# Kernel optimization log

Hardware: AMD Instinct MI355X
Metric: run time of the kernel (lower is better)

## Reference

```python
import jax, jax.numpy as jnp
import numpy as np

THETA = 10000.0

def _rope(t):
    # lucidrains-style interleaved rotary over the FULL last dim (dim=hidden_size)
    T, d = t.shape[-2], t.shape[-1]
    freqs = 1.0 / (THETA ** (jnp.arange(0, d, 2, dtype=jnp.float32) / d))  # (d/2,)
    ang = jnp.arange(T, dtype=jnp.float32)[:, None] * freqs[None, :]       # (T, d/2)
    ang = jnp.repeat(ang, 2, axis=-1)                                      # (T, d) interleaved
    cos, sin = jnp.cos(ang), jnp.sin(ang)
    x = t.reshape(t.shape[:-1] + (d // 2, 2))
    x1, x2 = x[..., 0], x[..., 1]
    rot = jnp.stack([-x2, x1], axis=-1).reshape(t.shape)  # rotate_half, interleaved pairs
    return t * cos + rot * sin


def setup_inputs() -> dict:
    key = jax.random.key(0)
    ks = jax.random.split(key, 5)
    B, T, C = 4, 2048, 1024
    s = 0.02
    return {
        "x":  jax.random.normal(ks[0], (B, T, C), dtype=jnp.float32),
        "Wq": jax.random.normal(ks[1], (C, C), dtype=jnp.float32) * s,
        "bq": jnp.zeros((C,), dtype=jnp.float32),
        "Wk": jax.random.normal(ks[2], (C, C), dtype=jnp.float32) * s,
        "bk": jnp.zeros((C,), dtype=jnp.float32),
        "Wv": jax.random.normal(ks[3], (C, C), dtype=jnp.float32) * s,
        "bv": jnp.zeros((C,), dtype=jnp.float32),
        "Wf": jax.random.normal(ks[4], (C, C), dtype=jnp.float32) * s,
        "bf": jnp.zeros((C,), dtype=jnp.float32),
    }


def reference(x, Wq, bq, Wk, bk, Wv, bv, Wf, bf):
    B, T, C = x.shape
    Q = _rope(x @ Wq.T + bq)
    K = _rope(x @ Wk.T + bk)
    V = x @ Wv.T + bv
    # scores [B,T,T]; _get_D(gamma=1, T) is exactly a causal lower-triangular mask
    A = jnp.einsum('btd,bsd->bts', Q, K) / jnp.sqrt(jnp.float32(C))
    causal = jnp.tril(jnp.ones((T, T), dtype=bool))
    A = jnp.where(causal, A, -jnp.inf)
    A = jax.nn.softmax(A, axis=-1)
    out = jnp.einsum('bts,bsd->btd', A, V)
    return out @ Wf.T + bf
```

## Files before the change

### kernel.cpp

```cpp
#include <hip/hip_runtime.h>
#include <math.h>


#define AS1(p) ((__attribute__((address_space(1))) void*)(p))
#define AS3(p) ((__attribute__((address_space(3))) void*)(p))

typedef __attribute__((ext_vector_type(8))) short bf16x8;
typedef __attribute__((ext_vector_type(4))) float f32x4;

__device__ __forceinline__ unsigned short f2bf(float f) {
  unsigned int u = __float_as_uint(f);
  u += 0x7fffu + ((u >> 16) & 1u);
  return (unsigned short)(u >> 16);
}

__global__ __launch_bounds__(256) void cast_all(
    const float* __restrict__ x, const float* __restrict__ Wq,
    const float* __restrict__ Wk, const float* __restrict__ Wv,
    const float* __restrict__ Wf,
    unsigned short* __restrict__ xb, unsigned short* __restrict__ Wqb,
    unsigned short* __restrict__ Wkb, unsigned short* __restrict__ Wvb,
    unsigned short* __restrict__ Wfb) {
  int i = blockIdx.x * 256 + threadIdx.x;
  const float* src; unsigned short* dst; int off;
  if (i < 2097152) { src = x; dst = xb; off = i; }
  else {
    int j = i - 2097152;
    int w = j >> 18; off = j & 262143;
    src = (w == 0) ? Wq : (w == 1) ? Wk : (w == 2) ? Wv : Wf;
    dst = (w == 0) ? Wqb : (w == 1) ? Wkb : (w == 2) ? Wvb : Wfb;
  }
  float4 f = ((const float4*)src)[off];
  ushort4 o;
  o.x = f2bf(f.x); o.y = f2bf(f.y); o.z = f2bf(f.z); o.w = f2bf(f.w);
  ((ushort4*)dst)[off] = o;
}

__device__ __forceinline__ void gemm_core(const unsigned short* __restrict__ At, long long lda,
                                          const unsigned short* __restrict__ Bt, long long ldb,
                                          int K, f32x4 (&acc)[4][4],
                                          unsigned short* As, unsigned short* Bs) {
  const int tid  = threadIdx.x;
  const int lane = tid & 63;
  const int w    = tid >> 6;
  const int wm   = (w & 1) << 6;
  const int wn   = (w >> 1) << 6;
  const int fr   = lane & 15;
  const int fq   = lane >> 4;
  const int srow = tid >> 2;
  const int scol = (tid & 3) << 3;
  const int lg   = ((tid & 3) ^ ((srow >> 1) & 3)) << 3;
  const unsigned short* a0 = At + (long long)srow * lda + lg;
  const unsigned short* a1 = At + (long long)(srow + 64) * lda + lg;
  const unsigned short* b0 = Bt + (long long)srow * ldb + lg;
  const unsigned short* b1 = Bt + (long long)(srow + 64) * ldb + lg;
  unsigned short* As0 = As + srow * 32 + scol;
  unsigned short* As1 = As + (srow + 64) * 32 + scol;
  unsigned short* Bs0 = Bs + srow * 32 + scol;
  unsigned short* Bs1 = Bs + (srow + 64) * 32 + scol;
  const int pg = (fq ^ ((fr >> 1) & 3)) << 3;
  for (int k0 = 0; k0 < K; k0 += 32) {
    __builtin_amdgcn_global_load_lds(AS1(a0 + k0), AS3(As0), 16, 0, 0);
    __builtin_amdgcn_global_load_lds(AS1(a1 + k0), AS3(As1), 16, 0, 0);
    __builtin_amdgcn_global_load_lds(AS1(b0 + k0), AS3(Bs0), 16, 0, 0);
    __builtin_amdgcn_global_load_lds(AS1(b1 + k0), AS3(Bs1), 16, 0, 0);
    __syncthreads();
    bf16x8 af[4], bfr[4];
#pragma unroll
    for (int i = 0; i < 4; i++)
      af[i] = *(const bf16x8*)(As + (wm + i * 16 + fr) * 32 + pg);
#pragma unroll
    for (int i = 0; i < 4; i++)
      bfr[i] = *(const bf16x8*)(Bs + (wn + i * 16 + fr) * 32 + pg);
#pragma unroll
    for (int mi = 0; mi < 4; mi++)
#pragma unroll
      for (int ni = 0; ni < 4; ni++)
        acc[mi][ni] = __builtin_amdgcn_mfma_f32_16x16x32_bf16(af[mi], bfr[ni], acc[mi][ni], 0, 0, 0);
    __syncthreads();
  }
}

__device__ __forceinline__ void repack_store_mi(unsigned short (&vals)[4][4],
                                                unsigned short* sh, int mi,
                                                int m0, int n0, long long ldo,
                                                unsigned short* __restrict__ Out) {
  const int tid = threadIdx.x, lane = tid & 63, w = tid >> 6;
  const int half = w & 1, wn = (w >> 1) << 6;
  const int cl = lane & 15, q4 = lane >> 4;
  const int lr = half * 16 + q4 * 4;
#pragma unroll
  for (int ni = 0; ni < 4; ni++)
#pragma unroll
    for (int rr = 0; rr < 4; rr++)
      sh[(lr + rr) * 132 + wn + ni * 16 + cl] = vals[ni][rr];
  __syncthreads();
#pragma unroll
  for (int it = 0; it < 2; ++it) {
    int row = (tid >> 4) + it * 16;
    int c8 = (tid & 15) << 3;
    bf16x8 v = *(const bf16x8*)(sh + row * 132 + c8);
    int gr = m0 + (row < 16 ? mi * 16 + row : 48 + mi * 16 + row);
    *(bf16x8*)(Out + (long long)gr * ldo + n0 + c8) = v;
  }
  __syncthreads();
}

__global__ __launch_bounds__(256) void proj_rope(
    const unsigned short* __restrict__ xb,
    const unsigned short* __restrict__ Wq, const unsigned short* __restrict__ Wk,
    const unsigned short* __restrict__ Wv,
    const float* __restrict__ bq, const float* __restrict__ bk, const float* __restrict__ bv,
    unsigned short* __restrict__ Q, unsigned short* __restrict__ Ko,
    unsigned short* __restrict__ Vt) {
  __shared__ unsigned short sh[8192];
  const int which = blockIdx.z;
  const int tid = threadIdx.x, lane = tid & 63, w = tid >> 6;
  const int wm = (w & 1) << 6, wn = (w >> 1) << 6;
  const int cl = lane & 15, q4 = lane >> 4;

  f32x4 acc[4][4];
#pragma unroll
  for (int i = 0; i < 4; i++)
#pragma unroll
    for (int j = 0; j < 4; j++)
#pragma unroll
      for (int k = 0; k < 4; k++) acc[i][j][k] = 0.0f;

  if (which == 2) {
    const int s0g = blockIdx.x * 128;
    const int d0 = blockIdx.y * 128;
    gemm_core(Wv + (long long)d0 * 1024, 1024, xb + (long long)s0g * 1024, 1024,
              1024, acc, sh, sh + 4096);
    const int b = s0g >> 11;
    const int sloc = s0g & 2047;
    unsigned short* Outb = Vt + (long long)b * 1024 * 2048;
#pragma unroll
    for (int mi = 0; mi < 4; mi++) {
      unsigned short vals[4][4];
#pragma unroll
      for (int rr = 0; rr < 4; rr++) {
        const float b_ = bv[d0 + wm + mi * 16 + q4 * 4 + rr];
#pragma unroll
        for (int ni = 0; ni < 4; ni++)
          vals[ni][rr] = f2bf(acc[mi][ni][rr] + b_);
      }
      repack_store_mi(vals, sh, mi, d0, sloc, 2048, Outb);
    }
    return;
  }

  const int m0 = blockIdx.x * 128;
  const int n0 = blockIdx.y * 128;
  const unsigned short* W = which == 0 ? Wq : Wk;
  const float* bias = which == 0 ? bq : bk;
  unsigned short* Out = which == 0 ? Q : Ko;

  gemm_core(xb + (long long)m0 * 1024, 1024, W + (long long)n0 * 1024, 1024, 1024, acc, sh, sh + 4096);

  const float NEG_L2T_512 = -0.025952563239354392f;
  const float INV2PI = 0.15915494309189535f;
  float freqn[4];
#pragma unroll
  for (int ni = 0; ni < 4; ni++) {
    int gn = n0 + wn + ni * 16 + cl;
    freqn[ni] = exp2f(NEG_L2T_512 * (float)(gn >> 1));
  }
#pragma unroll
  for (int mi = 0; mi < 4; mi++) {
    unsigned short vals[4][4];
    const int t0 = (m0 & 2047) + wm + mi * 16 + q4 * 4;
#pragma unroll
    for (int ni = 0; ni < 4; ni++) {
      const int gn = n0 + wn + ni * 16 + cl;
#pragma unroll
      for (int rr = 0; rr < 4; rr++) {
        float v = acc[mi][ni][rr] + bias[gn];
        float partner = __shfl_xor(v, 1, 64);
        float ang = (float)(t0 + rr) * freqn[ni];
        float rev = ang * INV2PI;
        rev = rev - floorf(rev);
        float c = __builtin_amdgcn_cosf(rev);
        float s = __builtin_amdgcn_sinf(rev);
        v = v * c + ((gn & 1) ? partner : -partner) * s;
        vals[ni][rr] = f2bf(v);
      }
    }
    repack_store_mi(vals, sh, mi, m0, n0, 1024, Out);
  }
}

__global__ __launch_bounds__(256) void score_exp(const unsigned short* __restrict__ Q,
                                                 const unsigned short* __restrict__ Kk,
                                                 unsigned short* __restrict__ P,
                                                 float* __restrict__ row_sum) {
  __shared__ unsigned short sh[8192];
  const int bx = blockIdx.x;
  int i = (int)((sqrtf(8.0f * (float)bx + 1.0f) - 1.0f) * 0.5f);
  while ((i + 1) * (i + 2) / 2 <= bx) ++i;
  while (i * (i + 1) / 2 > bx) --i;
  const int j = bx - i * (i + 1) / 2;
  const int b = blockIdx.z;
  const int m0 = i * 128, n0 = j * 128;
  const unsigned short* Qb = Q + (long long)b * 2048 * 1024;
  const unsigned short* Kb = Kk + (long long)b * 2048 * 1024;
  unsigned short* Pb = P + (long long)b * 2048 * 2048;
  float* rs = row_sum + b * 2048;

  f32x4 acc[4][4];
#pragma unroll
  for (int ii = 0; ii < 4; ii++)
#pragma unroll
    for (int jj = 0; jj < 4; jj++)
#pragma unroll
      for (int k = 0; k < 4; k++) acc[ii][jj][k] = 0.0f;

  gemm_core(Qb + (long long)m0 * 1024, 1024, Kb + (long long)n0 * 1024, 1024, 1024, acc, sh, sh + 4096);

  const int tid = threadIdx.x, lane = tid & 63, w = tid >> 6;
  const int wm = (w & 1) << 6, wn = (w >> 1) << 6;
  const int cl = lane & 15, q4 = lane >> 4;
  const bool diag = (i == j);
#pragma unroll
  for (int mi = 0; mi < 4; mi++) {
    unsigned short vals[4][4];
    float rsum[4] = {0.f, 0.f, 0.f, 0.f};
#pragma unroll
    for (int ni = 0; ni < 4; ni++) {
      const int gn = n0 + wn + ni * 16 + cl;
#pragma unroll
      for (int rr = 0; rr < 4; rr++) {
        const int gm = m0 + wm + mi * 16 + q4 * 4 + rr;
        float e = (diag && gn > gm) ? 0.0f : __expf(acc[mi][ni][rr] * 0.03125f);
        vals[ni][rr] = f2bf(e);
        rsum[rr] += e;
      }
    }
#pragma unroll
    for (int rr = 0; rr < 4; rr++) {
#pragma unroll
      for (int off = 1; off < 16; off <<= 1) rsum[rr] += __shfl_xor(rsum[rr], off, 64);
    }
    if (cl == 0) {
      const int gm = m0 + wm + mi * 16 + q4 * 4;
#pragma unroll
      for (int rr = 0; rr < 4; rr++) atomicAdd(&rs[gm + rr], rsum[rr]);
    }
    repack_store_mi(vals, sh, mi, m0, n0, 2048, Pb);
  }
}

__global__ __launch_bounds__(256) void pv_gemm(const unsigned short* __restrict__ P,
                                               const unsigned short* __restrict__ Vt,
                                               const float* __restrict__ row_sum,
                                               unsigned short* __restrict__ O) {
  __shared__ unsigned short sh[8192];
  const int b = blockIdx.z;
  const int mt = 15 - blockIdx.x;
  const int m0 = mt * 128;
  const int n0 = blockIdx.y * 128;
  const unsigned short* Pb = P + (long long)b * 2048 * 2048;
  const unsigned short* Vb = Vt + (long long)b * 1024 * 2048;
  const float* rs = row_sum + b * 2048;
  const int K = m0 + 128;

  f32x4 acc[4][4];
#pragma unroll
  for (int i = 0; i < 4; i++)
#pragma unroll
    for (int j = 0; j < 4; j++)
#pragma unroll
      for (int k = 0; k < 4; k++) acc[i][j][k] = 0.0f;

  gemm_core(Pb + (long long)m0 * 2048, 2048, Vb + (long long)n0 * 2048, 2048, K, acc, sh, sh + 4096);

  const int tid = threadIdx.x, lane = tid & 63, w = tid >> 6;
  const int wm = (w & 1) << 6;
  const int q4 = lane >> 4;
#pragma unroll
  for (int mi = 0; mi < 4; mi++) {
    unsigned short vals[4][4];
    float inv[4];
    const int gm0 = m0 + wm + mi * 16 + q4 * 4;
#pragma unroll
    for (int rr = 0; rr < 4; rr++) inv[rr] = 1.0f / rs[gm0 + rr];
#pragma unroll
    for (int ni = 0; ni < 4; ni++)
#pragma unroll
      for (int rr = 0; rr < 4; rr++)
        vals[ni][rr] = f2bf(acc[mi][ni][rr] * inv[rr]);
    repack_store_mi(vals, sh, mi, m0, n0, 1024, O + (long long)b * 2048 * 1024);
  }
}

__global__ __launch_bounds__(256) void final_gemm(const unsigned short* __restrict__ O,
                                                  const unsigned short* __restrict__ Wf,
                                                  const float* __restrict__ bf_,
                                                  float* __restrict__ out) {
  __shared__ unsigned short sh[8448];
  float* shf = (float*)sh;
  const int m0 = blockIdx.x * 128;
  const int n0 = blockIdx.y * 128;

  f32x4 acc[4][4];
#pragma unroll
  for (int i = 0; i < 4; i++)
#pragma unroll
    for (int j = 0; j < 4; j++)
#pragma unroll
      for (int k = 0; k < 4; k++) acc[i][j][k] = 0.0f;

  gemm_core(O + (long long)m0 * 1024, 1024, Wf + (long long)n0 * 1024, 1024, 1024, acc, sh, sh + 4096);

  const int tid = threadIdx.x, lane = tid & 63, w = tid >> 6;
  const int half = w & 1, wn = (w >> 1) << 6;
  const int cl = lane & 15, q4 = lane >> 4;
  const int lr = half * 16 + q4 * 4;
#pragma unroll
  for (int mi = 0; mi < 4; mi++) {
#pragma unroll
    for (int ni = 0; ni < 4; ni++)
#pragma unroll
      for (int rr = 0; rr < 4; rr++)
        shf[(lr + rr) * 130 + wn + ni * 16 + cl] = acc[mi][ni][rr] + bf_[n0 + wn + ni * 16 + cl];
    __syncthreads();
    {
      int row = tid >> 3;
      int c4 = (tid & 7) << 4;
      int gr = m0 + (row < 16 ? mi * 16 + row : 48 + mi * 16 + row);
      float* dst = out + (long long)gr * 1024 + n0 + c4;
      const float* srcp = shf + row * 130 + c4;
#pragma unroll
      for (int j = 0; j < 4; j++)
        ((float4*)dst)[j] = ((const float4*)srcp)[j];
    }
    __syncthreads();
  }
}

extern "C" void kernel_launch(void* const* d_in, const int* in_sizes, int n_in,
                              void* d_out, int out_size, void* d_ws, size_t ws_size,
                              hipStream_t stream) {
  (void)in_sizes; (void)n_in; (void)out_size; (void)ws_size;
  const float* x   = (const float*)d_in[0];
  const float* Wq  = (const float*)d_in[1];
  const float* bq  = (const float*)d_in[2];
  const float* Wk  = (const float*)d_in[3];
  const float* bk  = (const float*)d_in[4];
  const float* Wv  = (const float*)d_in[5];
  const float* bv  = (const float*)d_in[6];
  const float* Wf  = (const float*)d_in[7];
  const float* bf_ = (const float*)d_in[8];
  float* out = (float*)d_out;

  char* ws = (char*)d_ws;
  const size_t MB = 1024 * 1024;
  unsigned short* xb  = (unsigned short*)(ws);
  unsigned short* Wqb = (unsigned short*)(ws + 16 * MB);
  unsigned short* Wkb = (unsigned short*)(ws + 18 * MB);
  unsigned short* Wvb = (unsigned short*)(ws + 20 * MB);
  unsigned short* Wfb = (unsigned short*)(ws + 22 * MB);
  unsigned short* Qb  = (unsigned short*)(ws + 24 * MB);
  unsigned short* Kb  = (unsigned short*)(ws + 40 * MB);
  unsigned short* Vtb = (unsigned short*)(ws + 56 * MB);
  unsigned short* Ob  = (unsigned short*)(ws + 72 * MB);
  unsigned short* Pb  = (unsigned short*)(ws + 88 * MB);
  float*          rsum= (float*)(ws + 120 * MB);

  dim3 blk(256);
  hipMemsetAsync(rsum, 0, 8192 * sizeof(float), stream);
  cast_all<<<dim3(3145728 / 256), blk, 0, stream>>>(x, Wq, Wk, Wv, Wf, xb, Wqb, Wkb, Wvb, Wfb);
  proj_rope<<<dim3(64, 8, 3), blk, 0, stream>>>(xb, Wqb, Wkb, Wvb, bq, bk, bv, Qb, Kb, Vtb);
  score_exp<<<dim3(136, 1, 4), blk, 0, stream>>>(Qb, Kb, Pb, rsum);
  pv_gemm<<<dim3(16, 8, 4), blk, 0, stream>>>(Pb, Vtb, rsum, Ob);
  final_gemm<<<dim3(64, 8), blk, 0, stream>>>(Ob, Wfb, bf_, out);
}
```

Measured before the change: 299.1 us.

## Replace projection and output GEMM cores with 8-wave 128x256 pipelined core

Adds a new 512-thread GEMM core with 128x256 tiles, K-step 64, double-buffered direct global-to-LDS loads, XOR-swizzled LDS reads, and phased MFMA interleaving with setprio and barriers. The QKV projection and final output GEMM switch to it with larger tiles and new epilogues that stage results through LDS for coalesced stores. The aim is to raise MFMA utilisation and hide memory latency in these GEMMs. In exchange it uses much more LDS per block and many barriers, and it launches fewer blocks.

```diff
diff --git a/kernel.cpp b/kernel.cpp
--- a/kernel.cpp
+++ b/kernel.cpp
@@ -106,17 +106,134 @@
   __syncthreads();
 }
 
-__global__ __launch_bounds__(256) void proj_rope(
+__device__ __forceinline__ void core8(
+    const unsigned short* __restrict__ A, long long lda,
+    const unsigned short* __restrict__ B, long long ldb,
+    int nkt, f32x4 (&acc)[4][4], unsigned short* lds) {
+  const int tid  = threadIdx.x;
+  const int lane = tid & 63;
+  const int w    = tid >> 6;
+  const int wr   = w >> 2;
+  const int wc   = w & 3;
+  const int fr   = lane & 15;
+  const int fq   = lane >> 4;
+  const int rsw0 = (fq ^ (fr & 7)) << 3;
+  const int rsw1 = ((4 + fq) ^ (fr & 7)) << 3;
+  const int sr   = tid >> 3;
+  const int kswz = ((tid & 7) ^ (sr & 7)) << 3;
+  const unsigned short* Asrc = A + (long long)sr * lda + kswz;
+  const unsigned short* Bsrc = B + (long long)sr * ldb + kswz;
+  unsigned short* ldsw = lds + tid * 8;
+
+  auto stageA = [&](int b_, int kt_) {
+    const unsigned short* s0 = Asrc + (long long)kt_ * 64;
+    __builtin_amdgcn_global_load_lds(AS1(s0),            AS3(ldsw + b_ * 24576),         16, 0, 0);
+    __builtin_amdgcn_global_load_lds(AS1(s0 + 64 * lda), AS3(ldsw + b_ * 24576 + 4096),  16, 0, 0);
+  };
+  auto stageB = [&](int b_, int kt_) {
+    const unsigned short* s0 = Bsrc + (long long)kt_ * 64;
+    __builtin_amdgcn_global_load_lds(AS1(s0),             AS3(ldsw + b_ * 24576 + 8192),  16, 0, 0);
+    __builtin_amdgcn_global_load_lds(AS1(s0 + 64 * ldb),  AS3(ldsw + b_ * 24576 + 12288), 16, 0, 0);
+    __builtin_amdgcn_global_load_lds(AS1(s0 + 128 * ldb), AS3(ldsw + b_ * 24576 + 16384), 16, 0, 0);
+    __builtin_amdgcn_global_load_lds(AS1(s0 + 192 * ldb), AS3(ldsw + b_ * 24576 + 20480), 16, 0, 0);
+  };
+
+  stageA(0, 0); stageB(0, 0);
+  if (nkt > 1) {
+    stageA(1, 1); stageB(1, 1);
+    asm volatile("s_waitcnt vmcnt(6)" ::: "memory");
+  } else {
+    asm volatile("s_waitcnt vmcnt(0)" ::: "memory");
+  }
+  __builtin_amdgcn_s_barrier();
+
+  const unsigned short* Ar = lds + (wr * 64 + fr) * 64;
+  const unsigned short* Br = lds + 8192 + (wc * 64 + fr) * 64;
+
+#define MFMA2(ACC, A0, A1, B0, B1)                                            \
+  ACC = __builtin_amdgcn_mfma_f32_16x16x32_bf16(A0, B0, ACC, 0, 0, 0);        \
+  ACC = __builtin_amdgcn_mfma_f32_16x16x32_bf16(A1, B1, ACC, 0, 0, 0);
+
+#pragma unroll 1
+  for (int kt = 0; kt < nkt; ++kt) {
+    const int b = kt & 1;
+    const unsigned short* Ab = Ar + b * 24576;
+    const unsigned short* Bb = Br + b * 24576;
+    bf16x8 aL[4], aH[4], bE[4], bO[4];
+    aL[0] = *(const bf16x8*)(Ab + rsw0);
+    aL[1] = *(const bf16x8*)(Ab + rsw1);
+    aL[2] = *(const bf16x8*)(Ab + 1024 + rsw0);
+    aL[3] = *(const bf16x8*)(Ab + 1024 + rsw1);
+    bE[0] = *(const bf16x8*)(Bb + rsw0);
+    bE[1] = *(const bf16x8*)(Bb + rsw1);
+    bE[2] = *(const bf16x8*)(Bb + 1024 + rsw0);
+    bE[3] = *(const bf16x8*)(Bb + 1024 + rsw1);
+    __builtin_amdgcn_s_barrier();
+    asm volatile("s_waitcnt lgkmcnt(0)" ::: "memory");
+    __builtin_amdgcn_s_setprio(1);
+    MFMA2(acc[0][0], aL[0], aL[1], bE[0], bE[1]);
+    MFMA2(acc[0][1], aL[0], aL[1], bE[2], bE[3]);
+    MFMA2(acc[1][0], aL[2], aL[3], bE[0], bE[1]);
+    MFMA2(acc[1][1], aL[2], aL[3], bE[2], bE[3]);
+    __builtin_amdgcn_s_setprio(0);
+    __builtin_amdgcn_s_barrier();
+    bO[0] = *(const bf16x8*)(Bb + 2048 + rsw0);
+    bO[1] = *(const bf16x8*)(Bb + 2048 + rsw1);
+    bO[2] = *(const bf16x8*)(Bb + 3072 + rsw0);
+    bO[3] = *(const bf16x8*)(Bb + 3072 + rsw1);
+    __builtin_amdgcn_s_barrier();
+    asm volatile("s_waitcnt lgkmcnt(0)" ::: "memory");
+    __builtin_amdgcn_s_setprio(1);
+    MFMA2(acc[0][2], aL[0], aL[1], bO[0], bO[1]);
+    MFMA2(acc[0][3], aL[0], aL[1], bO[2], bO[3]);
+    MFMA2(acc[1][2], aL[2], aL[3], bO[0], bO[1]);
+    MFMA2(acc[1][3], aL[2], aL[3], bO[2], bO[3]);
+    __builtin_amdgcn_s_setprio(0);
+    __builtin_amdgcn_s_barrier();
+    aH[0] = *(const bf16x8*)(Ab + 2048 + rsw0);
+    aH[1] = *(const bf16x8*)(Ab + 2048 + rsw1);
+    aH[2] = *(const bf16x8*)(Ab + 3072 + rsw0);
+    aH[3] = *(const bf16x8*)(Ab + 3072 + rsw1);
+    if (kt + 2 < nkt) stageB(b, kt + 2);
+    __builtin_amdgcn_s_barrier();
+    asm volatile("s_waitcnt lgkmcnt(0)" ::: "memory");
+    __builtin_amdgcn_s_setprio(1);
+    MFMA2(acc[2][0], aH[0], aH[1], bE[0], bE[1]);
+    MFMA2(acc[2][1], aH[0], aH[1], bE[2], bE[3]);
+    MFMA2(acc[3][0], aH[2], aH[3], bE[0], bE[1]);
+    MFMA2(acc[3][1], aH[2], aH[3], bE[2], bE[3]);
+    __builtin_amdgcn_s_setprio(0);
+    __builtin_amdgcn_s_barrier();
+    if (kt + 2 < nkt) stageA(b, kt + 2);
+    if (kt + 1 < nkt) {
+      if (kt + 2 < nkt)
+        asm volatile("s_waitcnt vmcnt(6)" ::: "memory");
+      else
+        asm volatile("s_waitcnt vmcnt(0)" ::: "memory");
+    }
+    __builtin_amdgcn_s_barrier();
+    __builtin_amdgcn_s_setprio(1);
+    MFMA2(acc[2][2], aH[0], aH[1], bO[0], bO[1]);
+    MFMA2(acc[2][3], aH[0], aH[1], bO[2], bO[3]);
+    MFMA2(acc[3][2], aH[2], aH[3], bO[0], bO[1]);
+    MFMA2(acc[3][3], aH[2], aH[3], bO[2], bO[3]);
+    __builtin_amdgcn_s_setprio(0);
+    __builtin_amdgcn_s_barrier();
+  }
+#undef MFMA2
+}
+
+__global__ __launch_bounds__(512, 2) void proj_rope(
     const unsigned short* __restrict__ xb,
     const unsigned short* __restrict__ Wq, const unsigned short* __restrict__ Wk,
     const unsigned short* __restrict__ Wv,
     const float* __restrict__ bq, const float* __restrict__ bk, const float* __restrict__ bv,
     unsigned short* __restrict__ Q, unsigned short* __restrict__ Ko,
     unsigned short* __restrict__ Vt) {
-  __shared__ unsigned short sh[8192];
+  __shared__ unsigned short lds[49152];
   const int which = blockIdx.z;
   const int tid = threadIdx.x, lane = tid & 63, w = tid >> 6;
-  const int wm = (w & 1) << 6, wn = (w >> 1) << 6;
+  const int wr = w >> 2, wc = w & 3;
   const int cl = lane & 15, q4 = lane >> 4;
 
   f32x4 acc[4][4];
@@ -128,65 +245,81 @@
       for (int k = 0; k < 4; k++) acc[i][j][k] = 0.0f;
 
   if (which == 2) {
-    const int s0g = blockIdx.x * 128;
-    const int d0 = blockIdx.y * 128;
-    gemm_core(Wv + (long long)d0 * 1024, 1024, xb + (long long)s0g * 1024, 1024,
-              1024, acc, sh, sh + 4096);
-    const int b = s0g >> 11;
-    const int sloc = s0g & 2047;
+    const int flat = blockIdx.x * 4 + blockIdx.y;
+    const int m0 = (flat & 7) * 128;
+    const int n0 = (flat >> 3) * 256;
+    core8(Wv + (long long)m0 * 1024, 1024, xb + (long long)n0 * 1024, 1024, 16, acc, lds);
+    __syncthreads();
+    const int b = n0 >> 11, sloc = n0 & 2047;
+#pragma unroll
+    for (int mi = 0; mi < 4; ++mi) {
+      const int lr = wr * 64 + mi * 16 + q4 * 4;
+#pragma unroll
+      for (int rr = 0; rr < 4; ++rr) {
+        const float b_ = bv[m0 + lr + rr];
+#pragma unroll
+        for (int nj = 0; nj < 4; ++nj)
+          lds[(lr + rr) * 264 + wc * 64 + nj * 16 + cl] = f2bf(acc[mi][nj][rr] + b_);
+      }
+    }
+    __syncthreads();
     unsigned short* Outb = Vt + (long long)b * 1024 * 2048;
 #pragma unroll
-    for (int mi = 0; mi < 4; mi++) {
-      unsigned short vals[4][4];
-#pragma unroll
-      for (int rr = 0; rr < 4; rr++) {
-        const float b_ = bv[d0 + wm + mi * 16 + q4 * 4 + rr];
-#pragma unroll
-        for (int ni = 0; ni < 4; ni++)
-          vals[ni][rr] = f2bf(acc[mi][ni][rr] + b_);
-      }
-      repack_store_mi(vals, sh, mi, d0, sloc, 2048, Outb);
+    for (int it = 0; it < 8; ++it) {
+      int c = it * 512 + tid;
+      int row = c >> 5, c8 = (c & 31) << 3;
+      bf16x8 v = *(const bf16x8*)(lds + row * 264 + c8);
+      *(bf16x8*)(Outb + (long long)(m0 + row) * 2048 + sloc + c8) = v;
     }
     return;
   }
 
   const int m0 = blockIdx.x * 128;
-  const int n0 = blockIdx.y * 128;
+  const int n0 = blockIdx.y * 256;
   const unsigned short* W = which == 0 ? Wq : Wk;
   const float* bias = which == 0 ? bq : bk;
   unsigned short* Out = which == 0 ? Q : Ko;
 
-  gemm_core(xb + (long long)m0 * 1024, 1024, W + (long long)n0 * 1024, 1024, 1024, acc, sh, sh + 4096);
+  core8(xb + (long long)m0 * 1024, 1024, W + (long long)n0 * 1024, 1024, 16, acc, lds);
+  __syncthreads();
 
   const float NEG_L2T_512 = -0.025952563239354392f;
   const float INV2PI = 0.15915494309189535f;
   float freqn[4];
 #pragma unroll
-  for (int ni = 0; ni < 4; ni++) {
-    int gn = n0 + wn + ni * 16 + cl;
-    freqn[ni] = exp2f(NEG_L2T_512 * (float)(gn >> 1));
-  }
-#pragma unroll
-  for (int mi = 0; mi < 4; mi++) {
-    unsigned short vals[4][4];
-    const int t0 = (m0 & 2047) + wm + mi * 16 + q4 * 4;
-#pragma unroll
-    for (int ni = 0; ni < 4; ni++) {
-      const int gn = n0 + wn + ni * 16 + cl;
-#pragma unroll
-      for (int rr = 0; rr < 4; rr++) {
-        float v = acc[mi][ni][rr] + bias[gn];
+  for (int nj = 0; nj < 4; ++nj) {
+    int gn = n0 + wc * 64 + nj * 16 + cl;
+    freqn[nj] = exp2f(NEG_L2T_512 * (float)(gn >> 1));
+  }
+#pragma unroll
+  for (int mi = 0; mi < 4; ++mi) {
+    const int lr = wr * 64 + mi * 16 + q4 * 4;
+    const int t0 = (m0 & 2047) + lr;
+#pragma unroll
+    for (int nj = 0; nj < 4; ++nj) {
+      const int gn = n0 + wc * 64 + nj * 16 + cl;
+      const float bi = bias[gn];
+#pragma unroll
+      for (int rr = 0; rr < 4; ++rr) {
+        float v = acc[mi][nj][rr] + bi;
         float partner = __shfl_xor(v, 1, 64);
-        float ang = (float)(t0 + rr) * freqn[ni];
+        float ang = (float)(t0 + rr) * freqn[nj];
         float rev = ang * INV2PI;
         rev = rev - floorf(rev);
-        float c = __builtin_amdgcn_cosf(rev);
-        float s = __builtin_amdgcn_sinf(rev);
-        v = v * c + ((gn & 1) ? partner : -partner) * s;
-        vals[ni][rr] = f2bf(v);
+        float c_ = __builtin_amdgcn_cosf(rev);
+        float s_ = __builtin_amdgcn_sinf(rev);
+        v = v * c_ + ((gn & 1) ? partner : -partner) * s_;
+        lds[(lr + rr) * 264 + wc * 64 + nj * 16 + cl] = f2bf(v);
       }
     }
-    repack_store_mi(vals, sh, mi, m0, n0, 1024, Out);
+  }
+  __syncthreads();
+#pragma unroll
+  for (int it = 0; it < 8; ++it) {
+    int c = it * 512 + tid;
+    int row = c >> 5, c8 = (c & 31) << 3;
+    bf16x8 v = *(const bf16x8*)(lds + row * 264 + c8);
+    *(bf16x8*)(Out + (long long)(m0 + row) * 1024 + n0 + c8) = v;
   }
 }
 
@@ -293,14 +426,17 @@
   }
 }
 
-__global__ __launch_bounds__(256) void final_gemm(const unsigned short* __restrict__ O,
-                                                  const unsigned short* __restrict__ Wf,
-                                                  const float* __restrict__ bf_,
-                                                  float* __restrict__ out) {
-  __shared__ unsigned short sh[8448];
-  float* shf = (float*)sh;
+__global__ __launch_bounds__(512, 2) void final_gemm(const unsigned short* __restrict__ O,
+                                                     const unsigned short* __restrict__ Wf,
+                                                     const float* __restrict__ bf_,
+                                                     float* __restrict__ out) {
+  __shared__ unsigned short lds[49152];
+  float* shf = (float*)lds;
+  const int tid = threadIdx.x, lane = tid & 63, w = tid >> 6;
+  const int wr = w >> 2, wc = w & 3;
+  const int cl = lane & 15, q4 = lane >> 4;
   const int m0 = blockIdx.x * 128;
-  const int n0 = blockIdx.y * 128;
+  const int n0 = blockIdx.y * 256;
 
   f32x4 acc[4][4];
 #pragma unroll
@@ -310,31 +446,31 @@
 #pragma unroll
       for (int k = 0; k < 4; k++) acc[i][j][k] = 0.0f;
 
-  gemm_core(O + (long long)m0 * 1024, 1024, Wf + (long long)n0 * 1024, 1024, 1024, acc, sh, sh + 4096);
-
-  const int tid = threadIdx.x, lane = tid & 63, w = tid >> 6;
-  const int half = w & 1, wn = (w >> 1) << 6;
-  const int cl = lane & 15, q4 = lane >> 4;
-  const int lr = half * 16 + q4 * 4;
-#pragma unroll
-  for (int mi = 0; mi < 4; mi++) {
-#pragma unroll
-    for (int ni = 0; ni < 4; ni++)
-#pragma unroll
-      for (int rr = 0; rr < 4; rr++)
-        shf[(lr + rr) * 130 + wn + ni * 16 + cl] = acc[mi][ni][rr] + bf_[n0 + wn + ni * 16 + cl];
+  core8(O + (long long)m0 * 1024, 1024, Wf + (long long)n0 * 1024, 1024, 16, acc, lds);
+
+#pragma unroll
+  for (int r = 0; r < 2; ++r) {
     __syncthreads();
-    {
-      int row = tid >> 3;
-      int c4 = (tid & 7) << 4;
-      int gr = m0 + (row < 16 ? mi * 16 + row : 48 + mi * 16 + row);
-      float* dst = out + (long long)gr * 1024 + n0 + c4;
-      const float* srcp = shf + row * 130 + c4;
-#pragma unroll
-      for (int j = 0; j < 4; j++)
-        ((float4*)dst)[j] = ((const float4*)srcp)[j];
+    if (wr == r) {
+#pragma unroll
+      for (int mi = 0; mi < 4; ++mi)
+#pragma unroll
+        for (int nj = 0; nj < 4; ++nj) {
+          const int col = wc * 64 + nj * 16 + cl;
+          const float bi = bf_[n0 + col];
+#pragma unroll
+          for (int rr = 0; rr < 4; ++rr)
+            shf[(mi * 16 + q4 * 4 + rr) * 260 + col] = acc[mi][nj][rr] + bi;
+        }
     }
     __syncthreads();
+#pragma unroll
+    for (int it = 0; it < 8; ++it) {
+      int c = it * 512 + tid;
+      int row = c >> 6, c4 = (c & 63) << 2;
+      float4 v = *(const float4*)(shf + row * 260 + c4);
+      *(float4*)(out + (long long)(m0 + r * 64 + row) * 1024 + n0 + c4) = v;
+    }
   }
 }
 
@@ -367,11 +503,10 @@
   unsigned short* Pb  = (unsigned short*)(ws + 88 * MB);
   float*          rsum= (float*)(ws + 120 * MB);
 
-  dim3 blk(256);
   hipMemsetAsync(rsum, 0, 8192 * sizeof(float), stream);
-  cast_all<<<dim3(3145728 / 256), blk, 0, stream>>>(x, Wq, Wk, Wv, Wf, xb, Wqb, Wkb, Wvb, Wfb);
-  proj_rope<<<dim3(64, 8, 3), blk, 0, stream>>>(xb, Wqb, Wkb, Wvb, bq, bk, bv, Qb, Kb, Vtb);
-  score_exp<<<dim3(136, 1, 4), blk, 0, stream>>>(Qb, Kb, Pb, rsum);
-  pv_gemm<<<dim3(16, 8, 4), blk, 0, stream>>>(Pb, Vtb, rsum, Ob);
-  final_gemm<<<dim3(64, 8), blk, 0, stream>>>(Ob, Wfb, bf_, out);
-}
+  cast_all<<<dim3(3145728 / 256), dim3(256), 0, stream>>>(x, Wq, Wk, Wv, Wf, xb, Wqb, Wkb, Wvb, Wfb);
+  proj_rope<<<dim3(64, 4, 3), dim3(512), 0, stream>>>(xb, Wqb, Wkb, Wvb, bq, bk, bv, Qb, Kb, Vtb);
+  score_exp<<<dim3(136, 1, 4), dim3(256), 0, stream>>>(Qb, Kb, Pb, rsum);
+  pv_gemm<<<dim3(16, 8, 4), dim3(256), 0, stream>>>(Pb, Vtb, rsum, Ob);
+  final_gemm<<<dim3(64, 4), dim3(512), 0, stream>>>(Ob, Wfb, bf_, out);
+}
```

Result: faster. 293.0 us (-2.0%).
